# Performance work log

Hardware: AMD Instinct MI355X
Metric: run time of the kernel (lower is better)

Reference implementation:

```python
import jax, jax.numpy as jnp
import numpy as np

E = 8          # num_experts
K = 2          # top-k
H = 768        # hidden_size
F = 4 * H      # FFN intermediate (expansion_factor=4)
B, S = 2, 2048


def setup_inputs() -> dict:
    key = jax.random.key(0)
    ks = jax.random.split(key, 5)
    scale = 0.02
    return {
        "x": jax.random.normal(ks[0], (B, S, H), dtype=jnp.float32),
        "router_w": jax.random.normal(ks[1], (H, E), dtype=jnp.float32) * scale,
        "router_b": jnp.zeros((E,), dtype=jnp.float32),
        "w1": jax.random.normal(ks[2], (E, H, F), dtype=jnp.float32) * scale,
        "b1": jnp.zeros((E, F), dtype=jnp.float32),
        "w2": jax.random.normal(ks[3], (E, F, H), dtype=jnp.float32) * scale,
        "b2": jnp.zeros((E, H), dtype=jnp.float32),
    }


def reference(x, router_w, router_b, w1, b1, w2, b2):
    b, s, h = x.shape
    # Router
    scores = jnp.einsum("bsh,he->bse", x, router_w) + router_b
    probs = jax.nn.softmax(scores, axis=-1)                      # [b,s,E]
    top_probs, expert_ids = jax.lax.top_k(probs, K)              # [b,s,K]

    # Load-balance auxiliary loss (Switch-style)
    avg_probs = probs.mean(axis=(0, 1))                          # [E]
    top1 = jnp.argmax(probs, axis=-1).reshape(-1)                # [b*s]
    counts = jnp.zeros((E,), dtype=probs.dtype).at[top1].add(1.0)
    expert_freqs = counts / (b * s)
    bal_loss = 0.001 * jnp.dot(expert_freqs, avg_probs)

    # Normalize top-k gate weights
    norm_probs = top_probs / (top_probs.sum(axis=-1, keepdims=True) + 1e-9)  # [b,s,K]

    # Expert FFNs with ReLU^2 activation, computed per-expert (dense, then masked)
    h1 = jnp.einsum("bsh,ehf->ebsf", x, w1) + b1[:, None, None, :]
    h1 = jnp.square(jax.nn.relu(h1))
    h2 = jnp.einsum("ebsf,efh->ebsh", h1, w2) + b2[:, None, None, :]  # [E,b,s,H]

    # Combine: weight for expert e at token (b,s) = sum_k norm_probs * 1[ids_k == e]
    onehot = jax.nn.one_hot(expert_ids, E, dtype=x.dtype)        # [b,s,K,E]
    gate = jnp.einsum("bsk,bske->ebs", norm_probs, onehot)       # [E,b,s]
    out = jnp.einsum("ebs,ebsh->bsh", gate, h2)                  # [b,s,H]
    return out, bal_loss
```

## Files before the change

kernel.cpp:

```cpp
#include <hip/hip_runtime.h>
#include <hip/hip_bf16.h>
#include <stdint.h>

#define E_EXP 8
#define TOK   4096
#define HD    768
#define FD    3072
#define BK    64
#define CAP   8320
#define NKP2  2

typedef __attribute__((ext_vector_type(8))) short bf16x8;
typedef __attribute__((ext_vector_type(4))) float f32x4;

__device__ __forceinline__ unsigned short f2bf(float f) {
  union { float f; unsigned u; } v; v.f = f;
  unsigned r = v.u + 0x7fffu + ((v.u >> 16) & 1u);
  return (unsigned short)(r >> 16);
}
__device__ __forceinline__ float bf2f(unsigned short u) {
  union { unsigned u; float f; } v; v.u = ((unsigned)u) << 16;
  return v.f;
}

__device__ __forceinline__ void gload_lds16(const void* g, void* l) {
  __builtin_amdgcn_global_load_lds(
      (const __attribute__((address_space(1))) unsigned int*)g,
      (__attribute__((address_space(3))) unsigned int*)l, 16, 0, 0);
}

__device__ __forceinline__ int xcd_swizzle(int orig, int nwg) {
  int xcd = orig & 7, base = orig >> 3;
  int q = nwg >> 3, r = nwg & 7;
  return (xcd < r ? xcd * (q + 1) : r * (q + 1) + (xcd - r) * q) + base;
}

#define TT 64
#define T1_TILES (E_EXP * (FD / TT) * (HD / TT))
#define T2_TILES (E_EXP * (HD / TT) * (FD / TT))
#define ROUTER_BLOCKS (TOK / 4)
__global__ __launch_bounds__(256) void prep_kernel(
    const float* __restrict__ x, const float* __restrict__ rw,
    const float* __restrict__ rb, unsigned short* __restrict__ xb,
    float* __restrict__ probs, int* __restrict__ ids,
    float* __restrict__ gates,
    const float* __restrict__ w1, unsigned short* __restrict__ w1t,
    const float* __restrict__ w2, unsigned short* __restrict__ w2t)
{
  __shared__ union {
    float lrw[E_EXP * HD];
    unsigned short tile[TT][TT + 4];
  } sh;

  if (blockIdx.x < ROUTER_BLOCKS) {
    for (int i = threadIdx.x; i < E_EXP * HD; i += 256) {
      int h = i >> 3, e = i & 7;
      sh.lrw[e * HD + h] = rw[i];
    }
    __syncthreads();
    const int wave = threadIdx.x >> 6, lane = threadIdx.x & 63;
    const int t = blockIdx.x * 4 + wave;
    const float* xrow = x + (size_t)t * HD;
    float acc[8] = {0, 0, 0, 0, 0, 0, 0, 0};
#pragma unroll
    for (int i = 0; i < HD / 64; ++i) {
      int h = i * 64 + lane;
      float xv = xrow[h];
      xb[(size_t)t * HD + h] = f2bf(xv);
#pragma unroll
      for (int e = 0; e < 8; ++e) acc[e] += xv * sh.lrw[e * HD + h];
    }
#pragma unroll
    for (int d = 1; d < 64; d <<= 1) {
#pragma unroll
      for (int e = 0; e < 8; ++e) acc[e] += __shfl_xor(acc[e], d);
    }
    if (lane == 0) {
      float p[8]; float m = -1e30f, sum = 0.f;
#pragma unroll
      for (int e = 0; e < 8; ++e) { p[e] = acc[e] + rb[e]; m = fmaxf(m, p[e]); }
#pragma unroll
      for (int e = 0; e < 8; ++e) { p[e] = __expf(p[e] - m); sum += p[e]; }
      float inv = 1.f / sum;
#pragma unroll
      for (int e = 0; e < 8; ++e) p[e] *= inv;
      int i1 = 0;
#pragma unroll
      for (int e = 1; e < 8; ++e) if (p[e] > p[i1]) i1 = e;
      int i2 = (i1 == 0) ? 1 : 0;
#pragma unroll
      for (int e = 0; e < 8; ++e) if (e != i1 && p[e] > p[i2]) i2 = e;
      ids[t * 2] = i1; ids[t * 2 + 1] = i2;
      float den = 1.f / (p[i1] + p[i2] + 1e-9f);
      gates[t * 2] = p[i1] * den; gates[t * 2 + 1] = p[i2] * den;
#pragma unroll
      for (int e = 0; e < 8; ++e) probs[t * 8 + e] = p[e];
    }
    return;
  }

  int id = blockIdx.x - ROUTER_BLOCKS;
  const float* W; unsigned short* Wt; int Kd, Nd;
  if (id < T1_TILES) {
    W = w1; Wt = w1t; Kd = HD; Nd = FD;
  } else {
    id -= T1_TILES; W = w2; Wt = w2t; Kd = FD; Nd = HD;
  }
  const int nx = Nd / TT, nk = Kd / TT;
  const int e = id / (nx * nk);
  const int rem = id % (nx * nk);
  const int n0 = (rem % nx) * TT, k0 = (rem / nx) * TT;

  const int r0 = threadIdx.x >> 4;
  const int c4 = threadIdx.x & 15;
#pragma unroll
  for (int i = 0; i < 4; ++i) {
    int kk = r0 + i * 16;
    float4 v = *(const float4*)&W[((size_t)e * Kd + k0 + kk) * Nd + n0 + c4 * 4];
    sh.tile[c4 * 4 + 0][kk] = f2bf(v.x);
    sh.tile[c4 * 4 + 1][kk] = f2bf(v.y);
    sh.tile[c4 * 4 + 2][kk] = f2bf(v.z);
    sh.tile[c4 * 4 + 3][kk] = f2bf(v.w);
  }
  __syncthreads();
  const int n = threadIdx.x >> 2, kc = threadIdx.x & 3;
  unsigned short* dst = Wt + ((size_t)e * Nd + n0 + n) * Kd + k0 + kc * 16;
  bf16x8 a = *(const bf16x8*)&sh.tile[n][kc * 16];
  bf16x8 b = *(const bf16x8*)&sh.tile[n][kc * 16 + 8];
  *(bf16x8*)&dst[0] = a;
  *(bf16x8*)&dst[8] = b;
}

__global__ __launch_bounds__(1024) void stats_scatter_kernel(
    const int* __restrict__ ids, const float* __restrict__ probs,
    int* __restrict__ meta, int* __restrict__ token_list,
    int* __restrict__ pos_list, float* __restrict__ loss_out)
{
  __shared__ int cnt[8], top1c[8], cur[8];
  __shared__ float wsum[16][8];
  const int tid = threadIdx.x;
  if (tid < 8) { cnt[tid] = 0; top1c[tid] = 0; cur[tid] = 0; }
  __syncthreads();
  float local[8] = {0, 0, 0, 0, 0, 0, 0, 0};
  for (int t = tid; t < TOK; t += 1024) {
    int e0 = ids[2 * t], e1 = ids[2 * t + 1];
    atomicAdd(&cnt[e0], 1); atomicAdd(&cnt[e1], 1); atomicAdd(&top1c[e0], 1);
    const float4* pr = (const float4*)&probs[(size_t)t * 8];
    float4 a = pr[0], b = pr[1];
    local[0] += a.x; local[1] += a.y; local[2] += a.z; local[3] += a.w;
    local[4] += b.x; local[5] += b.y; local[6] += b.z; local[7] += b.w;
  }
#pragma unroll
  for (int d = 1; d < 64; d <<= 1) {
#pragma unroll
    for (int e = 0; e < 8; ++e) local[e] += __shfl_xor(local[e], d);
  }
  const int wave = tid >> 6, lane = tid & 63;
  if (lane == 0) {
#pragma unroll
    for (int e = 0; e < 8; ++e) wsum[wave][e] = local[e];
  }
  __syncthreads();
  if (tid == 0) {
    int total = 0, nt1 = 0;
    for (int e = 0; e < 8; ++e) {
      int c = cnt[e];
      meta[e] = c;
      meta[16 + e] = total;
      int t1 = (c + 127) >> 7;
      for (int i = 0; i < t1; ++i) { meta[64 + nt1 * 2] = e; meta[64 + nt1 * 2 + 1] = total + i * 128; ++nt1; }
      total += c;
    }
    meta[32] = nt1;
    float loss = 0.f;
    for (int e = 0; e < 8; ++e) {
      float psum = 0.f;
      for (int w = 0; w < 16; ++w) psum += wsum[w][e];
      loss += ((float)top1c[e] / 4096.f) * (psum / 4096.f);
    }
    loss_out[0] = 0.001f * loss;
  }
  __syncthreads();
  for (int t = tid; t < TOK; t += 1024) {
    int e0 = ids[2 * t], e1 = ids[2 * t + 1];
    int s0 = atomicAdd(&cur[e0], 1);
    int s1 = atomicAdd(&cur[e1], 1);
    int p0 = meta[16 + e0] + s0;
    int p1 = meta[16 + e1] + s1;
    token_list[p0] = t; pos_list[2 * t] = p0;
    token_list[p1] = t; pos_list[2 * t + 1] = p1;
  }
}

template<int BM, int BN, int MODE, int NW, int NKP>
__global__ __launch_bounds__(NW * 64, 4) void moe_gemm(
    const unsigned short* __restrict__ A,
    const unsigned short* __restrict__ Bw,
    const float* __restrict__ bias,
    const int* __restrict__ token_list,
    const int* __restrict__ meta,
    unsigned short* __restrict__ Cout,
    const int Kdim, const int NN)
{
  const int NY = NN / BN;
  const int wgid = xcd_swizzle(blockIdx.x, gridDim.x);
  const int mt = wgid / (NY * NKP);
  const int slot = wgid - mt * (NY * NKP);
  const int ny = slot % NY;
  const int kp = slot / NY;
  const int nt_total = meta[32];
  if (mt >= nt_total) return;
  const int* tmap = meta + 64;
  const int e = tmap[mt * 2], arow0 = tmap[mt * 2 + 1];
  const int ne_end = meta[16 + e] + meta[e];
  const int n0 = ny * BN;
  const int KLEN = Kdim / NKP;
  const int kbeg = kp * KLEN;
  unsigned short* Cp = Cout + (size_t)kp * CAP * NN;

  __shared__ unsigned short lA[BM * BK];
  __shared__ unsigned short lB[BN * BK];

  const int tid = threadIdx.x;
  const int wave = tid >> 6, lane = tid & 63;
  constexpr int WC_N = NW / 2;
  const int wr = wave / WC_N, wc = wave % WC_N;
  constexpr int WROWS = BM / 2;
  constexpr int WCOLS = BN / WC_N;
  constexpr int FM = WROWS / 16, FN = WCOLS / 16;
  constexpr int NCA = (BM / 8) / NW;
  constexpr int NCB = (BN / 8) / NW;

  const int kswz = ((lane & 7) ^ ((lane >> 3) & 7)) * 8;

  size_t aSrc[NCA];
#pragma unroll
  for (int i = 0; i < NCA; ++i) {
    int c = wave + i * NW;
    int r = c * 8 + (lane >> 3);
    int grow = (MODE == 0) ? token_list[arow0 + r] : (arow0 + r);
    aSrc[i] = (size_t)grow * Kdim + kbeg + kswz;
  }
  size_t bSrc[NCB];
#pragma unroll
  for (int i = 0; i < NCB; ++i) {
    int c = wave + i * NW;
    int n = n0 + c * 8 + (lane >> 3);
    bSrc[i] = ((size_t)e * NN + n) * Kdim + kbeg + kswz;
  }

  f32x4 acc[FM][FN] = {};

  for (int k0 = 0; k0 < KLEN; k0 += BK) {
#pragma unroll
    for (int i = 0; i < NCA; ++i)
      gload_lds16(A + aSrc[i] + k0, &lA[(wave + i * NW) * 512]);
#pragma unroll
    for (int i = 0; i < NCB; ++i)
      gload_lds16(Bw + bSrc[i] + k0, &lB[(wave + i * NW) * 512]);
    __syncthreads();
#pragma unroll
    for (int kk = 0; kk < BK; kk += 32) {
      bf16x8 af[FM], bfr[FN];
      const int lc = (kk >> 3) + (lane >> 4);
#pragma unroll
      for (int m2 = 0; m2 < FM; ++m2) {
        int row = wr * WROWS + m2 * 16 + (lane & 15);
        af[m2] = *(const bf16x8*)&lA[row * BK + ((lc ^ (row & 7)) << 3)];
      }
#pragma unroll
      for (int n2 = 0; n2 < FN; ++n2) {
        int row = wc * WCOLS + n2 * 16 + (lane & 15);
        bfr[n2] = *(const bf16x8*)&lB[row * BK + ((lc ^ (row & 7)) << 3)];
      }
#pragma unroll
      for (int m2 = 0; m2 < FM; ++m2)
#pragma unroll
        for (int n2 = 0; n2 < FN; ++n2)
          acc[m2][n2] = __builtin_amdgcn_mfma_f32_16x16x32_bf16(
              af[m2], bfr[n2], acc[m2][n2], 0, 0, 0);
    }
    __syncthreads();
  }

  const float* be = bias + (size_t)e * NN;
#pragma unroll
  for (int m2 = 0; m2 < FM; ++m2) {
    const int lr = wr * WROWS + m2 * 16 + (lane >> 4) * 4;
#pragma unroll
    for (int n2 = 0; n2 < FN; ++n2) {
      const int col = n0 + wc * WCOLS + n2 * 16 + (lane & 15);
      const float bv = (kp == 0) ? be[col] : 0.f;
#pragma unroll
      for (int j = 0; j < 4; ++j) {
        const int arow = arow0 + lr + j;
        if (arow < ne_end) {
          float v = acc[m2][n2][j] + bv;
          if (MODE == 0) { v = fmaxf(v, 0.f); v = v * v; }
          Cp[(size_t)arow * NN + col] = f2bf(v);
        }
      }
    }
  }
}

__global__ __launch_bounds__(256) void combine_kernel(
    const unsigned short* __restrict__ h2, const int* __restrict__ pos_list,
    const float* __restrict__ gates, float* __restrict__ out)
{
  const int wave = threadIdx.x >> 6, lane = threadIdx.x & 63;
  const int t = blockIdx.x * 4 + wave;
  const int p0 = pos_list[2 * t], p1 = pos_list[2 * t + 1];
  const float g0 = gates[2 * t], g1 = gates[2 * t + 1];
  float* o = out + (size_t)t * HD;
#pragma unroll
  for (int i = 0; i < 3; ++i) {
    int h = i * 256 + lane * 4;
    float4 o4 = {0.f, 0.f, 0.f, 0.f};
#pragma unroll
    for (int kp = 0; kp < NKP2; ++kp) {
      const unsigned short* base = h2 + (size_t)kp * CAP * HD;
      ushort4 a = *(const ushort4*)&base[(size_t)p0 * HD + h];
      ushort4 b = *(const ushort4*)&base[(size_t)p1 * HD + h];
      o4.x += g0 * bf2f(a.x) + g1 * bf2f(b.x);
      o4.y += g0 * bf2f(a.y) + g1 * bf2f(b.y);
      o4.z += g0 * bf2f(a.z) + g1 * bf2f(b.z);
      o4.w += g0 * bf2f(a.w) + g1 * bf2f(b.w);
    }
    *(float4*)&o[h] = o4;
  }
}

extern "C" void kernel_launch(void* const* d_in, const int* in_sizes, int n_in,
                              void* d_out, int out_size, void* d_ws, size_t ws_size,
                              hipStream_t stream)
{
  (void)in_sizes; (void)n_in; (void)ws_size; (void)out_size;
  const float* x  = (const float*)d_in[0];
  const float* rw = (const float*)d_in[1];
  const float* rb = (const float*)d_in[2];
  const float* w1 = (const float*)d_in[3];
  const float* b1 = (const float*)d_in[4];
  const float* w2 = (const float*)d_in[5];
  const float* b2 = (const float*)d_in[6];
  float* out = (float*)d_out;

  char* ws = (char*)d_ws;
  size_t off = 0;
  auto alloc = [&](size_t bytes) {
    off = (off + 255) & ~(size_t)255;
    void* p = ws + off;
    off += bytes;
    return p;
  };
  unsigned short* xb  = (unsigned short*)alloc((size_t)TOK * HD * 2);
  unsigned short* w1t = (unsigned short*)alloc((size_t)E_EXP * FD * HD * 2);
  unsigned short* w2t = (unsigned short*)alloc((size_t)E_EXP * HD * FD * 2);
  unsigned short* h1  = (unsigned short*)alloc((size_t)CAP * FD * 2);
  unsigned short* h2  = (unsigned short*)alloc((size_t)NKP2 * CAP * HD * 2);
  int*   token_list = (int*)alloc(CAP * 4);
  int*   pos_list   = (int*)alloc((size_t)TOK * 2 * 4);
  int*   ids        = (int*)alloc((size_t)TOK * 2 * 4);
  float* gates      = (float*)alloc((size_t)TOK * 2 * 4);
  float* probs      = (float*)alloc((size_t)TOK * 8 * 4);
  int*   meta       = (int*)alloc(1024 * 4);
  char*  ctrl       = (char*)token_list;
  size_t ctrl_bytes = (ws + off) - ctrl;

  hipMemsetAsync(ctrl, 0, ctrl_bytes, stream);

  prep_kernel<<<ROUTER_BLOCKS + T1_TILES + T2_TILES, 256, 0, stream>>>(
      x, rw, rb, xb, probs, ids, gates, w1, w1t, w2, w2t);
  stats_scatter_kernel<<<1, 1024, 0, stream>>>(ids, probs, meta,
      token_list, pos_list, out + (size_t)TOK * HD);
  moe_gemm<128, 128, 0, 4, 1><<<71 * (FD / 128), 256, 0, stream>>>(
      xb, w1t, b1, token_list, meta, h1, HD, FD);
  moe_gemm<128, 128, 1, 4, NKP2><<<71 * (HD / 128) * NKP2, 256, 0, stream>>>(
      h1, w2t, b2, token_list, meta, h2, FD, HD);
  combine_kernel<<<TOK / 4, 256, 0, stream>>>(h2, pos_list, gates, out);
}
```

Before: 191.2 us.

## Shrink prep kernel LDS, read router weights directly, pack transposed bf16 stores

The router blocks no longer stage the 24KB router weight matrix in shared memory. Each lane now reads two float4 values of router weights straight from global memory, so the shared allocation shrinks to the transpose tile only, which lets more blocks fit per CU. The weight transpose loads four consecutive k rows per thread and writes packed 64-bit bf16 groups to LDS instead of scattered 16-bit stores, and router blocks are moved to the end of the grid. The cost is repeated global or L2 reads of router weights by every wave.

```diff
diff --git a/kernel.cpp b/kernel.cpp
--- a/kernel.cpp
+++ b/kernel.cpp
@@ -47,19 +47,11 @@
     const float* __restrict__ w1, unsigned short* __restrict__ w1t,
     const float* __restrict__ w2, unsigned short* __restrict__ w2t)
 {
-  __shared__ union {
-    float lrw[E_EXP * HD];
-    unsigned short tile[TT][TT + 4];
-  } sh;
-
-  if (blockIdx.x < ROUTER_BLOCKS) {
-    for (int i = threadIdx.x; i < E_EXP * HD; i += 256) {
-      int h = i >> 3, e = i & 7;
-      sh.lrw[e * HD + h] = rw[i];
-    }
-    __syncthreads();
+  __shared__ unsigned short tile[TT][TT + 4];
+
+  if (blockIdx.x >= T1_TILES + T2_TILES) {
     const int wave = threadIdx.x >> 6, lane = threadIdx.x & 63;
-    const int t = blockIdx.x * 4 + wave;
+    const int t = (blockIdx.x - (T1_TILES + T2_TILES)) * 4 + wave;
     const float* xrow = x + (size_t)t * HD;
     float acc[8] = {0, 0, 0, 0, 0, 0, 0, 0};
 #pragma unroll
@@ -67,8 +59,12 @@
       int h = i * 64 + lane;
       float xv = xrow[h];
       xb[(size_t)t * HD + h] = f2bf(xv);
-#pragma unroll
-      for (int e = 0; e < 8; ++e) acc[e] += xv * sh.lrw[e * HD + h];
+      const float4* rp = (const float4*)&rw[h * 8];
+      float4 r0 = rp[0], r1 = rp[1];
+      acc[0] += xv * r0.x; acc[1] += xv * r0.y;
+      acc[2] += xv * r0.z; acc[3] += xv * r0.w;
+      acc[4] += xv * r1.x; acc[5] += xv * r1.y;
+      acc[6] += xv * r1.z; acc[7] += xv * r1.w;
     }
 #pragma unroll
     for (int d = 1; d < 64; d <<= 1) {
@@ -99,7 +95,7 @@
     return;
   }
 
-  int id = blockIdx.x - ROUTER_BLOCKS;
+  int id = blockIdx.x;
   const float* W; unsigned short* Wt; int Kd, Nd;
   if (id < T1_TILES) {
     W = w1; Wt = w1t; Kd = HD; Nd = FD;
@@ -111,22 +107,29 @@
   const int rem = id % (nx * nk);
   const int n0 = (rem % nx) * TT, k0 = (rem / nx) * TT;
 
-  const int r0 = threadIdx.x >> 4;
-  const int c4 = threadIdx.x & 15;
-#pragma unroll
-  for (int i = 0; i < 4; ++i) {
-    int kk = r0 + i * 16;
-    float4 v = *(const float4*)&W[((size_t)e * Kd + k0 + kk) * Nd + n0 + c4 * 4];
-    sh.tile[c4 * 4 + 0][kk] = f2bf(v.x);
-    sh.tile[c4 * 4 + 1][kk] = f2bf(v.y);
-    sh.tile[c4 * 4 + 2][kk] = f2bf(v.z);
-    sh.tile[c4 * 4 + 3][kk] = f2bf(v.w);
+  const int c4 = threadIdx.x & 15, kq = threadIdx.x >> 4;
+  float4 v[4];
+#pragma unroll
+  for (int j2 = 0; j2 < 4; ++j2) {
+    int k = kq * 4 + j2;
+    v[j2] = *(const float4*)&W[((size_t)e * Kd + k0 + k) * Nd + n0 + c4 * 4];
+  }
+  const float* vf = (const float*)v;
+#pragma unroll
+  for (int j = 0; j < 4; ++j) {
+    int row = c4 * 4 + j;
+    unsigned long long pk =
+        (unsigned long long)f2bf(vf[0 * 4 + j]) |
+        ((unsigned long long)f2bf(vf[1 * 4 + j]) << 16) |
+        ((unsigned long long)f2bf(vf[2 * 4 + j]) << 32) |
+        ((unsigned long long)f2bf(vf[3 * 4 + j]) << 48);
+    *(unsigned long long*)&tile[row][kq * 4] = pk;
   }
   __syncthreads();
   const int n = threadIdx.x >> 2, kc = threadIdx.x & 3;
   unsigned short* dst = Wt + ((size_t)e * Nd + n0 + n) * Kd + k0 + kc * 16;
-  bf16x8 a = *(const bf16x8*)&sh.tile[n][kc * 16];
-  bf16x8 b = *(const bf16x8*)&sh.tile[n][kc * 16 + 8];
+  bf16x8 a = *(const bf16x8*)&tile[n][kc * 16];
+  bf16x8 b = *(const bf16x8*)&tile[n][kc * 16 + 8];
   *(bf16x8*)&dst[0] = a;
   *(bf16x8*)&dst[8] = b;
 }
@@ -369,7 +372,7 @@
 
   hipMemsetAsync(ctrl, 0, ctrl_bytes, stream);
 
-  prep_kernel<<<ROUTER_BLOCKS + T1_TILES + T2_TILES, 256, 0, stream>>>(
+  prep_kernel<<<T1_TILES + T2_TILES + ROUTER_BLOCKS, 256, 0, stream>>>(
       x, rw, rb, xb, probs, ids, gates, w1, w1t, w2, w2t);
   stats_scatter_kernel<<<1, 1024, 0, stream>>>(ids, probs, meta,
       token_list, pos_list, out + (size_t)TOK * HD);
```

After: 193.7 us. About the same (+1.3%).
